# Kernel tuning notes

Measured on AMD Instinct MI355X. Metric: run time of the kernel, lower is better.

Reference implementation:

```python
import jax, jax.numpy as jnp
import numpy as np

# Tsit5 Butcher tableau (Tsitouras 2011), b7 = 0 for the accepted solution.
_C = (0.161, 0.327, 0.9, 0.9800255409045097, 1.0)
_A = (
    (0.161,),
    (-0.008480655492356989, 0.335480655492357),
    (2.8971530571054935, -6.359448489975075, 4.3622954328695815),
    (5.325864828439257, -11.748883564062828, 7.4955393428898365, -0.09249506636175525),
    (5.86145544294642, -12.92096931784711, 8.159367898576159, -0.071584973281401, -0.028269050394068383),
)
_B = (0.09646076681806523, 0.01, 0.4798896504144996, 1.379008574103742, -3.290069515436081, 2.324710524099774)

K_STEPS, BATCH, N_STATE, N_INPUT, HIDDEN = 512, 64, 128, 32, 256


def setup_inputs() -> dict:
    key = jax.random.key(0)
    k1, k2, k3, k4 = jax.random.split(key, 4)
    ts = jnp.linspace(0.0, 1.0, K_STEPS, dtype=jnp.float32)
    y0 = jax.random.normal(k1, (BATCH, N_STATE), dtype=jnp.float32)
    us = jax.random.normal(k2, (BATCH, K_STEPS, N_INPUT), dtype=jnp.float32)
    fan_in = 1 + N_STATE + N_INPUT  # t, y, u
    W1 = jax.random.normal(k3, (HIDDEN, fan_in), dtype=jnp.float32) / np.sqrt(fan_in)
    b1 = jnp.zeros((HIDDEN,), dtype=jnp.float32)
    W2 = jax.random.normal(k4, (N_STATE, HIDDEN), dtype=jnp.float32) / np.sqrt(HIDDEN)
    b2 = jnp.zeros((N_STATE,), dtype=jnp.float32)
    return {"ts": ts, "y0": y0, "us": us, "W1": W1, "b1": b1, "W2": W2, "b2": b2}


def _solve(ts, y0_i, us_i, W1, b1, W2, b2):
    """Integrate one trajectory with fixed-step Tsit5 on the save grid."""
    dt_grid = jnp.diff(ts)                              # (k-1,)
    # backward-Hermite derivative estimates for the input signal u(t)
    d = jnp.diff(us_i, axis=0) / dt_grid[:, None]       # (k-1, m)
    d = jnp.concatenate([d[:1], d], axis=0)             # (k, m)

    def func(t, y, u):
        z = jnp.concatenate([t[None], y, u])
        return W2 @ jnp.tanh(W1 @ z + b1) + b2

    def u_at(i, theta):
        # cubic Hermite interpolation of u on interval [ts[i], ts[i+1]]
        h = dt_grid[i]
        u0, u1, d0, d1 = us_i[i], us_i[i + 1], d[i], d[i + 1]
        t2 = theta * theta
        t3 = t2 * theta
        return ((2 * t3 - 3 * t2 + 1) * u0 + (t3 - 2 * t2 + theta) * h * d0
                + (-2 * t3 + 3 * t2) * u1 + (t3 - t2) * h * d1)

    def step(y, i):
        t0, h = ts[i], dt_grid[i]
        ks = []
        k = func(t0, y, u_at(i, jnp.float32(0.0)))
        ks.append(k)
        for c, arow in zip(_C, _A):
            ytmp = y + h * sum(a * kj for a, kj in zip(arow, ks))
            ks.append(func(t0 + c * h, ytmp, u_at(i, jnp.float32(c))))
        y_new = y + h * sum(b * kj for b, kj in zip(_B, ks))
        return y_new, y_new

    _, ys = jax.lax.scan(step, y0_i, jnp.arange(ts.shape[0] - 1))
    return jnp.concatenate([y0_i[None], ys], axis=0)    # (k, n)


def reference(ts, y0, us, W1, b1, W2, b2):
    return jax.vmap(_solve, in_axes=(None, 0, 0, None, None, None, None))(
        ts, y0, us, W1, b1, W2, b2
    )
```

## Files before the change

### kernel.cpp

```cpp
#include <hip/hip_runtime.h>

namespace {

typedef _Float16 h2 __attribute__((ext_vector_type(2)));

constexpr int KSTEPS = 512;
constexpr int NSTATE = 128;
constexpr int NINPUT = 32;
constexpr int HID    = 256;
constexpr int FANIN  = 161;
constexpr int BATCH  = 64;
constexpr int CHUNK  = 64;
constexpr int NCH    = 8;

constexpr size_t WS_M  = 0;
constexpr size_t WS_C  = WS_M + (size_t)HID * HID * 2;
constexpr size_t WS_US = WS_C + HID * 4;
constexpr size_t WS_HB = WS_US + (size_t)BATCH * KSTEPS * NINPUT * 2;
constexpr size_t WS_T  = WS_HB + (size_t)BATCH * KSTEPS * HID * 2;

__device__ __forceinline__ float fdot2(h2 a, h2 b, float c) {
#if __has_builtin(__builtin_amdgcn_fdot2)
  return __builtin_amdgcn_fdot2(a, b, c, false);
#else
  return c + (float)a[0] * (float)b[0] + (float)a[1] * (float)b[1];
#endif
}

__device__ __forceinline__ float fast_tanh(float x) {
  float e2 = __builtin_amdgcn_exp2f(x * 2.8853900817779268f);
  float r  = __builtin_amdgcn_rcpf(e2 + 1.0f);
  return __builtin_fmaf(-2.0f, r, 1.0f);
}

template <int CTRL>
__device__ __forceinline__ float dpp_add(float x) {
  int y = __builtin_amdgcn_update_dpp(0, __float_as_int(x), CTRL, 0xF, 0xF, false);
  return x + __int_as_float(y);
}
__device__ __forceinline__ float red8(float x) {
  x = dpp_add<0xB1>(x);
  x = dpp_add<0x4E>(x);
  x = dpp_add<0x141>(x);
  return x;
}

#define BAR() __asm__ volatile("s_waitcnt lgkmcnt(0)\n\ts_barrier" ::: "memory")

union F4 { float4 f; h2 h[4]; };

__global__ __launch_bounds__(256)
void k1_compose(const float* __restrict__ W1, const float* __restrict__ W2,
                const float* __restrict__ b2, _Float16* __restrict__ wsM,
                float* __restrict__ wsC) {
  const int j  = blockIdx.x;
  const int hc = threadIdx.x;
  const float* w1row = W1 + (size_t)j * FANIN + 1;
  float acc = 0.0f;
  for (int o = 0; o < NSTATE; ++o)
    acc = __builtin_fmaf(w1row[o], W2[(size_t)o * HID + hc], acc);
  wsM[(size_t)j * HID + hc] = (_Float16)acc;
  if (hc == 0) {
    float ca = 0.0f;
    for (int o = 0; o < NSTATE; ++o) ca = __builtin_fmaf(w1row[o], b2[o], ca);
    wsC[j] = ca;
  }
}

__global__ __launch_bounds__(256)
void k1b_transcode(const float* __restrict__ us, _Float16* __restrict__ us16) {
  const size_t idx = ((size_t)blockIdx.x * 256 + threadIdx.x) * 4;
  const float4 v = *(const float4*)(us + idx);
  us16[idx + 0] = (_Float16)v.x;
  us16[idx + 1] = (_Float16)v.y;
  us16[idx + 2] = (_Float16)v.z;
  us16[idx + 3] = (_Float16)v.w;
}

__global__ __launch_bounds__(256)
__attribute__((amdgpu_waves_per_eu(1, 1)))
void k2_main(const float* __restrict__ ts,
             const float* __restrict__ y0,
             const float* __restrict__ W1,
             const float* __restrict__ b1,
             char* __restrict__ ws)
{
  const int lt = threadIdx.x;
  const int g  = lt >> 3;
  const int kc = lt & 7;
  const int b  = blockIdx.x;

  const _Float16* wsM  = (const _Float16*)(ws + WS_M);
  const float*    wsC  = (const float*)(ws + WS_C);
  const _Float16* us16 = (const _Float16*)(ws + WS_US) + (size_t)b * KSTEPS * NINPUT;
  _Float16*       wsHB = (_Float16*)(ws + WS_HB) + (size_t)b * KSTEPS * HID;
  float*          wsT  = (float*)(ws + WS_T) + (size_t)b * NCH * HID;

  __shared__ __align__(16) _Float16 hbuf[2][320];
  __shared__ __align__(16) float y0s[NSTATE];
  __shared__ __align__(16) float tss[KSTEPS];
  __shared__ __align__(16) _Float16 usl[KSTEPS * NINPUT];

  {
    const F4* src = (const F4*)us16;
    F4* dst = (F4*)usl;
    #pragma unroll
    for (int it = 0; it < 8; ++it) dst[lt + 256 * it] = src[lt + 256 * it];
    tss[lt] = ts[lt];
    tss[lt + 256] = ts[lt + 256];
  }

  h2 w1m[8][16];
  #pragma unroll
  for (int r = 0; r < 8; ++r) {
    const F4* mp = (const F4*)(wsM + (size_t)(8 * g + r) * HID + 32 * kc);
    F4 m0 = mp[0], m1 = mp[1], m2 = mp[2], m3 = mp[3];
    #pragma unroll
    for (int i = 0; i < 4; ++i) {
      w1m[r][i]      = m0.h[i];
      w1m[r][4 + i]  = m1.h[i];
      w1m[r][8 + i]  = m2.h[i];
      w1m[r][12 + i] = m3.h[i];
    }
  }
  const float* w1row = W1 + (size_t)lt * FANIN;
  const float  w1t   = w1row[0];
  h2 w1u[16];
  #pragma unroll
  for (int i = 0; i < 16; ++i)
    w1u[i] = h2{(_Float16)w1row[129 + 2 * i], (_Float16)w1row[130 + 2 * i]};
  const float cR = wsC[lt];

  if (lt < NSTATE) y0s[lt] = y0[(size_t)b * NSTATE + lt];
  __syncthreads();
  float P = b1[lt];
  {
    const float* wy = w1row + 1;
    #pragma unroll 8
    for (int o = 0; o < NSTATE; ++o) P = __builtin_fmaf(wy[o], y0s[o], P);
  }

  constexpr double CcD[5] = {0.161, 0.327, 0.9, 0.9800255409045097, 1.0};
  constexpr float Af[5][5] = {
    {0.161f, 0.f, 0.f, 0.f, 0.f},
    {-0.008480655492356989f, 0.335480655492357f, 0.f, 0.f, 0.f},
    {2.8971530571054935f, -6.359448489975075f, 4.3622954328695815f, 0.f, 0.f},
    {5.325864828439257f, -11.748883564062828f, 7.4955393428898365f, -0.09249506636175525f, 0.f},
    {5.86145544294642f, -12.92096931784711f, 8.159367898576159f, -0.071584973281401f,
     -0.028269050394068383f}};
  constexpr float Bf[6] = {0.09646076681806523f, 0.01f, 0.4798896504144996f,
                           1.379008574103742f, -3.290069515436081f, 2.324710524099774f};

  float Ua, Ub = 0.0f, Uaprev = 0.0f, D = 0.0f;
  {
    const F4* up = (const F4*)(usl);
    F4 u0 = up[0], u1 = up[1], u2 = up[2], u3 = up[3];
    float s = 0.0f;
    #pragma unroll
    for (int i = 0; i < 4; ++i) {
      s = fdot2(w1u[i],      u0.h[i], s);
      s = fdot2(w1u[4 + i],  u1.h[i], s);
      s = fdot2(w1u[8 + i],  u2.h[i], s);
      s = fdot2(w1u[12 + i], u3.h[i], s);
    }
    Ua = s;
  }

  float tcur = ts[0], tn1 = ts[1];
  float dtp = 1.0f;
  const int slot = 40 * (lt >> 5) + (lt & 31);
  float h0v = fast_tanh(P + Ua + w1t * tcur);
  hbuf[0][slot] = (_Float16)h0v;
  float hB = Bf[0] * h0v;
  float Sacc = 0.0f;
  float aR[6];

  for (int i = 0; i < KSTEPS - 1; ++i) {
    const float dt = tn1 - tcur;
    const int   i2 = (i + 2 < KSTEPS) ? (i + 2) : (KSTEPS - 1);
    const float tn2 = tss[i2];
    F4 ur0, ur1, ur2, ur3;
    {
      const F4* up = (const F4*)(&usl[(i + 1) * NINPUT]);
      ur0 = up[0]; ur1 = up[1]; ur2 = up[2]; ur3 = up[3];
    }

    if (i > 0 && (i & (CHUNK - 1)) == 0)
      wsT[(size_t)(i >> 6) * HID + lt] = Sacc;

    #pragma unroll
    for (int e = 0; e < 6; ++e) {
      BAR();

      const F4* hp = (const F4*)(&hbuf[e & 1][40 * kc]);
      F4 hc0 = hp[0], hc1 = hp[1], hc2 = hp[2], hc3 = hp[3];

      if (e == 5) {
        wsHB[(size_t)i * HID + lt] = (_Float16)hB;
      }
      if (e == 0) {
        float s = 0.0f;
        #pragma unroll
        for (int q = 0; q < 4; ++q) {
          s = fdot2(w1u[q],      ur0.h[q], s);
          s = fdot2(w1u[4 + q],  ur1.h[q], s);
          s = fdot2(w1u[8 + q],  ur2.h[q], s);
          s = fdot2(w1u[12 + q], ur3.h[q], s);
        }
        Ub = s;
        D = (i == 0) ? (Ub - Ua)
                     : (Ua - Uaprev) * (dt * __builtin_amdgcn_rcpf(dtp));
      }

      float acc[8];
      #pragma unroll
      for (int r = 0; r < 8; ++r) {
        float a0 = fdot2(w1m[r][0], hc0.h[0], 0.0f);
        float a1 = fdot2(w1m[r][1], hc0.h[1], 0.0f);
        a0 = fdot2(w1m[r][2],  hc0.h[2], a0);
        a1 = fdot2(w1m[r][3],  hc0.h[3], a1);
        a0 = fdot2(w1m[r][4],  hc1.h[0], a0);
        a1 = fdot2(w1m[r][5],  hc1.h[1], a1);
        a0 = fdot2(w1m[r][6],  hc1.h[2], a0);
        a1 = fdot2(w1m[r][7],  hc1.h[3], a1);
        a0 = fdot2(w1m[r][8],  hc2.h[0], a0);
        a1 = fdot2(w1m[r][9],  hc2.h[1], a1);
        a0 = fdot2(w1m[r][10], hc2.h[2], a0);
        a1 = fdot2(w1m[r][11], hc2.h[3], a1);
        a0 = fdot2(w1m[r][12], hc3.h[0], a0);
        a1 = fdot2(w1m[r][13], hc3.h[1], a1);
        a0 = fdot2(w1m[r][14], hc3.h[2], a0);
        a1 = fdot2(w1m[r][15], hc3.h[3], a1);
        acc[r] = a0 + a1;
      }
      #pragma unroll
      for (int r = 0; r < 8; ++r) acc[r] = red8(acc[r]);
      float ae = acc[0];
      #pragma unroll
      for (int r = 1; r < 8; ++r) ae = (kc == r) ? acc[r] : ae;
      ae += cR;
      aR[e] = ae;

      if (e < 5) {
        float acm = 0.0f;
        #pragma unroll
        for (int mm = 0; mm <= e; ++mm) acm = __builtin_fmaf(Af[e][mm], aR[mm], acm);
        const double th = CcD[e];
        const float cu0 = (float)(th * th * th - 2.0 * th * th + 1.0);
        const float cu1 = (float)(2.0 * th * th - th * th * th);
        const float cd0 = (float)(th * th * th - 2.0 * th * th + th);
        const float ut  = cu0 * Ua + cu1 * Ub + cd0 * D;
        const float te  = __builtin_fmaf((float)th, dt, tcur);
        float pre = __builtin_fmaf(dt, acm, P) + ut;
        pre = __builtin_fmaf(w1t, te, pre);
        const float hv = fast_tanh(pre);
        hbuf[(e + 1) & 1][slot] = (_Float16)hv;
        hB = __builtin_fmaf(Bf[e + 1], hv, hB);
      } else {
        float acm = 0.0f;
        #pragma unroll
        for (int mm = 0; mm < 6; ++mm) acm = __builtin_fmaf(Bf[mm], aR[mm], acm);
        P = __builtin_fmaf(dt, acm, P);
        Sacc = __builtin_fmaf(dt, hB, Sacc);
        float pre = P + Ub;
        pre = __builtin_fmaf(w1t, tn1, pre);
        const float hv = fast_tanh(pre);
        hbuf[0][slot] = (_Float16)hv;
        hB = Bf[0] * hv;
      }
    }

    Uaprev = Ua; Ua = Ub;
    dtp = dt; tcur = tn1; tn1 = tn2;
  }
}

__global__ __launch_bounds__(256, 1)
void k4_out(const float* __restrict__ ts,
            const float* __restrict__ y0,
            const float* __restrict__ W2,
            const char* __restrict__ ws,
            float* __restrict__ out)
{
  const int blk = blockIdx.x;
  const int b = blk >> 3;
  const int c = blk & 7;
  const int lt = threadIdx.x;
  const int o    = lt >> 1;
  const int half = lt & 1;

  const _Float16* wsHB = (const _Float16*)(ws + WS_HB) + (size_t)b * KSTEPS * HID;
  const float*    wsT  = (const float*)(ws + WS_T) + (size_t)b * NCH * HID;
  float* outb = out + (size_t)b * KSTEPS * NSTATE;

  __shared__ __align__(16) _Float16 Sb[HID];

  h2 w2r[64];
  {
    const float* row = W2 + (size_t)o * HID + 128 * half;
    #pragma unroll
    for (int i = 0; i < 64; ++i)
      w2r[i] = h2{(_Float16)row[2 * i], (_Float16)row[2 * i + 1]};
  }
  const float y0o = y0[(size_t)b * NSTATE + o];
  if (c == 0 && lt < NSTATE) outb[lt] = y0[(size_t)b * NSTATE + lt];

  float S = (c > 0) ? wsT[(size_t)c * HID + lt] : 0.0f;
  const int i0 = c * CHUNK;
  const int n  = (KSTEPS - 1 - i0 < CHUNK) ? (KSTEPS - 1 - i0) : CHUNK;

  float tc = ts[i0], tn = ts[i0 + 1];
  float hcur = (float)wsHB[(size_t)i0 * HID + lt];
  for (int l = 0; l < n; ++l) {
    const int i = i0 + l;
    const int inx = (i + 1 < KSTEPS - 1) ? (i + 1) : (KSTEPS - 2);
    const float hnext = (float)wsHB[(size_t)inx * HID + lt];
    const float tnn = ts[(i + 2 < KSTEPS) ? (i + 2) : (KSTEPS - 1)];

    const float dt = tn - tc;
    S = __builtin_fmaf(dt, hcur, S);
    Sb[lt] = (_Float16)S;
    __syncthreads();

    const F4* sp = (const F4*)(&Sb[128 * half]);
    float v0 = 0.0f, v1 = 0.0f;
    #pragma unroll
    for (int q = 0; q < 16; ++q) {
      F4 sc = sp[q];
      v0 = fdot2(w2r[4 * q + 0], sc.h[0], v0);
      v1 = fdot2(w2r[4 * q + 1], sc.h[1], v1);
      v0 = fdot2(w2r[4 * q + 2], sc.h[2], v0);
      v1 = fdot2(w2r[4 * q + 3], sc.h[3], v1);
    }
    float v = v0 + v1;
    v += __shfl_xor(v, 1);
    if (half == 0) outb[(size_t)(i + 1) * NSTATE + o] = y0o + v;
    __syncthreads();

    hcur = hnext; tc = tn; tn = tnn;
  }
}

}

extern "C" void kernel_launch(void* const* d_in, const int* in_sizes, int n_in,
                              void* d_out, int out_size, void* d_ws, size_t ws_size,
                              hipStream_t stream) {
  const float* ts = (const float*)d_in[0];
  const float* y0 = (const float*)d_in[1];
  const float* us = (const float*)d_in[2];
  const float* W1 = (const float*)d_in[3];
  const float* b1 = (const float*)d_in[4];
  const float* W2 = (const float*)d_in[5];
  const float* b2 = (const float*)d_in[6];
  float* out = (float*)d_out;
  char* ws = (char*)d_ws;

  _Float16* wsM  = (_Float16*)(ws + WS_M);
  float*    wsC  = (float*)(ws + WS_C);
  _Float16* us16 = (_Float16*)(ws + WS_US);

  hipLaunchKernelGGL(k1_compose, dim3(HID), dim3(HID), 0, stream, W1, W2, b2, wsM, wsC);
  hipLaunchKernelGGL(k1b_transcode, dim3(BATCH * KSTEPS * NINPUT / 1024), dim3(256),
                     0, stream, us, us16);
  hipLaunchKernelGGL(k2_main, dim3(BATCH), dim3(256), 0, stream, ts, y0, W1, b1, ws);
  hipLaunchKernelGGL(k4_out, dim3(BATCH * NCH), dim3(256), 0, stream, ts, y0, W2,
                     (const char*)ws, out);
}
```

Before: 1.573 ms.

## Replace fdot2 matvec and DPP reduction with MFMA 16x16x32 f16 tiles

The per-stage 256x256 hidden-to-hidden matvec is moved from packed fdot2 dot products plus an 8-lane DPP reduction onto MFMA 16x16x32 f16 instructions. Each wave keeps four 16-row A tiles of the composed matrix in registers and broadcasts the hidden vector as the B operand. Thread-to-hidden-unit mapping is remapped so each lane extracts its own output element from the accumulator without a cross-lane reduction. This wastes 15 of 16 MFMA columns, since only one vector is multiplied, and the MFMA latency sits on the serial critical path between barriers.

After: 1.546 ms. Within noise of the previous version (-1.7%).

```diff
diff --git a/kernel.cpp b/kernel.cpp
--- a/kernel.cpp
+++ b/kernel.cpp
@@ -3,6 +3,8 @@
 namespace {
 
 typedef _Float16 h2 __attribute__((ext_vector_type(2)));
+typedef _Float16 f16x8 __attribute__((ext_vector_type(8)));
+typedef float    f32x4 __attribute__((ext_vector_type(4)));
 
 constexpr int KSTEPS = 512;
 constexpr int NSTATE = 128;
@@ -31,18 +33,6 @@
   float e2 = __builtin_amdgcn_exp2f(x * 2.8853900817779268f);
   float r  = __builtin_amdgcn_rcpf(e2 + 1.0f);
   return __builtin_fmaf(-2.0f, r, 1.0f);
-}
-
-template <int CTRL>
-__device__ __forceinline__ float dpp_add(float x) {
-  int y = __builtin_amdgcn_update_dpp(0, __float_as_int(x), CTRL, 0xF, 0xF, false);
-  return x + __int_as_float(y);
-}
-__device__ __forceinline__ float red8(float x) {
-  x = dpp_add<0xB1>(x);
-  x = dpp_add<0x4E>(x);
-  x = dpp_add<0x141>(x);
-  return x;
 }
 
 #define BAR() __asm__ volatile("s_waitcnt lgkmcnt(0)\n\ts_barrier" ::: "memory")
@@ -86,8 +76,10 @@
              char* __restrict__ ws)
 {
   const int lt = threadIdx.x;
-  const int g  = lt >> 3;
-  const int kc = lt & 7;
+  const int w  = lt >> 6;
+  const int ln = lt & 63;
+  const int klo = ((ln >> 4) & 3) * 8;
+  const int j  = 64 * w + 16 * ((ln >> 2) & 3) + 4 * (ln >> 4) + (ln & 3);
   const int b  = blockIdx.x;
 
   const _Float16* wsM  = (const _Float16*)(ws + WS_M);
@@ -96,7 +88,7 @@
   _Float16*       wsHB = (_Float16*)(ws + WS_HB) + (size_t)b * KSTEPS * HID;
   float*          wsT  = (float*)(ws + WS_T) + (size_t)b * NCH * HID;
 
-  __shared__ __align__(16) _Float16 hbuf[2][320];
+  __shared__ __align__(16) _Float16 hbuf[2][HID];
   __shared__ __align__(16) float y0s[NSTATE];
   __shared__ __align__(16) float tss[KSTEPS];
   __shared__ __align__(16) _Float16 usl[KSTEPS * NINPUT];
@@ -110,30 +102,26 @@
     tss[lt + 256] = ts[lt + 256];
   }
 
-  h2 w1m[8][16];
+  f16x8 af[4][8];
   #pragma unroll
-  for (int r = 0; r < 8; ++r) {
-    const F4* mp = (const F4*)(wsM + (size_t)(8 * g + r) * HID + 32 * kc);
-    F4 m0 = mp[0], m1 = mp[1], m2 = mp[2], m3 = mp[3];
-    #pragma unroll
-    for (int i = 0; i < 4; ++i) {
-      w1m[r][i]      = m0.h[i];
-      w1m[r][4 + i]  = m1.h[i];
-      w1m[r][8 + i]  = m2.h[i];
-      w1m[r][12 + i] = m3.h[i];
-    }
-  }
-  const float* w1row = W1 + (size_t)lt * FANIN;
+  for (int t = 0; t < 4; ++t) {
+    const int row = 64 * w + 16 * t + (ln & 15);
+    #pragma unroll
+    for (int kk = 0; kk < 8; ++kk)
+      af[t][kk] = *(const f16x8*)(wsM + (size_t)row * HID + kk * 32 + klo);
+  }
+
+  const float* w1row = W1 + (size_t)j * FANIN;
   const float  w1t   = w1row[0];
   h2 w1u[16];
   #pragma unroll
   for (int i = 0; i < 16; ++i)
     w1u[i] = h2{(_Float16)w1row[129 + 2 * i], (_Float16)w1row[130 + 2 * i]};
-  const float cR = wsC[lt];
+  const float cR = wsC[j];
 
   if (lt < NSTATE) y0s[lt] = y0[(size_t)b * NSTATE + lt];
   __syncthreads();
-  float P = b1[lt];
+  float P = b1[j];
   {
     const float* wy = w1row + 1;
     #pragma unroll 8
@@ -168,9 +156,8 @@
 
   float tcur = ts[0], tn1 = ts[1];
   float dtp = 1.0f;
-  const int slot = 40 * (lt >> 5) + (lt & 31);
   float h0v = fast_tanh(P + Ua + w1t * tcur);
-  hbuf[0][slot] = (_Float16)h0v;
+  hbuf[0][j] = (_Float16)h0v;
   float hB = Bf[0] * h0v;
   float Sacc = 0.0f;
   float aR[6];
@@ -186,17 +173,14 @@
     }
 
     if (i > 0 && (i & (CHUNK - 1)) == 0)
-      wsT[(size_t)(i >> 6) * HID + lt] = Sacc;
+      wsT[(size_t)(i >> 6) * HID + j] = Sacc;
 
     #pragma unroll
     for (int e = 0; e < 6; ++e) {
       BAR();
 
-      const F4* hp = (const F4*)(&hbuf[e & 1][40 * kc]);
-      F4 hc0 = hp[0], hc1 = hp[1], hc2 = hp[2], hc3 = hp[3];
-
       if (e == 5) {
-        wsHB[(size_t)i * HID + lt] = (_Float16)hB;
+        wsHB[(size_t)i * HID + j] = (_Float16)hB;
       }
       if (e == 0) {
         float s = 0.0f;
@@ -212,32 +196,31 @@
                      : (Ua - Uaprev) * (dt * __builtin_amdgcn_rcpf(dtp));
       }
 
-      float acc[8];
+      const _Float16* hb = hbuf[e & 1];
+      f32x4 ac0 = {0.f, 0.f, 0.f, 0.f};
+      f32x4 ac1 = {0.f, 0.f, 0.f, 0.f};
+      f32x4 ac2 = {0.f, 0.f, 0.f, 0.f};
+      f32x4 ac3 = {0.f, 0.f, 0.f, 0.f};
       #pragma unroll
-      for (int r = 0; r < 8; ++r) {
-        float a0 = fdot2(w1m[r][0], hc0.h[0], 0.0f);
-        float a1 = fdot2(w1m[r][1], hc0.h[1], 0.0f);
-        a0 = fdot2(w1m[r][2],  hc0.h[2], a0);
-        a1 = fdot2(w1m[r][3],  hc0.h[3], a1);
-        a0 = fdot2(w1m[r][4],  hc1.h[0], a0);
-        a1 = fdot2(w1m[r][5],  hc1.h[1], a1);
-        a0 = fdot2(w1m[r][6],  hc1.h[2], a0);
-        a1 = fdot2(w1m[r][7],  hc1.h[3], a1);
-        a0 = fdot2(w1m[r][8],  hc2.h[0], a0);
-        a1 = fdot2(w1m[r][9],  hc2.h[1], a1);
-        a0 = fdot2(w1m[r][10], hc2.h[2], a0);
-        a1 = fdot2(w1m[r][11], hc2.h[3], a1);
-        a0 = fdot2(w1m[r][12], hc3.h[0], a0);
-        a1 = fdot2(w1m[r][13], hc3.h[1], a1);
-        a0 = fdot2(w1m[r][14], hc3.h[2], a0);
-        a1 = fdot2(w1m[r][15], hc3.h[3], a1);
-        acc[r] = a0 + a1;
-      }
-      #pragma unroll
-      for (int r = 0; r < 8; ++r) acc[r] = red8(acc[r]);
-      float ae = acc[0];
-      #pragma unroll
-      for (int r = 1; r < 8; ++r) ae = (kc == r) ? acc[r] : ae;
+      for (int kk = 0; kk < 8; ++kk) {
+        const f16x8 bf = *(const f16x8*)(hb + kk * 32 + klo);
+        ac0 = __builtin_amdgcn_mfma_f32_16x16x32_f16(af[0][kk], bf, ac0, 0, 0, 0);
+        ac1 = __builtin_amdgcn_mfma_f32_16x16x32_f16(af[1][kk], bf, ac1, 0, 0, 0);
+        ac2 = __builtin_amdgcn_mfma_f32_16x16x32_f16(af[2][kk], bf, ac2, 0, 0, 0);
+        ac3 = __builtin_amdgcn_mfma_f32_16x16x32_f16(af[3][kk], bf, ac3, 0, 0, 0);
+      }
+      float ae;
+      {
+        const bool b0 = (ln & 1) != 0;
+        const bool b1s = (ln & 2) != 0;
+        float e0 = b1s ? (b0 ? ac0[3] : ac0[2]) : (b0 ? ac0[1] : ac0[0]);
+        float e1 = b1s ? (b0 ? ac1[3] : ac1[2]) : (b0 ? ac1[1] : ac1[0]);
+        float e2 = b1s ? (b0 ? ac2[3] : ac2[2]) : (b0 ? ac2[1] : ac2[0]);
+        float e3 = b1s ? (b0 ? ac3[3] : ac3[2]) : (b0 ? ac3[1] : ac3[0]);
+        const bool t0 = (ln & 4) != 0;
+        const bool t1 = (ln & 8) != 0;
+        ae = t1 ? (t0 ? e3 : e2) : (t0 ? e1 : e0);
+      }
       ae += cR;
       aR[e] = ae;
 
@@ -254,7 +237,7 @@
         float pre = __builtin_fmaf(dt, acm, P) + ut;
         pre = __builtin_fmaf(w1t, te, pre);
         const float hv = fast_tanh(pre);
-        hbuf[(e + 1) & 1][slot] = (_Float16)hv;
+        hbuf[(e + 1) & 1][j] = (_Float16)hv;
         hB = __builtin_fmaf(Bf[e + 1], hv, hB);
       } else {
         float acm = 0.0f;
@@ -265,7 +248,7 @@
         float pre = P + Ub;
         pre = __builtin_fmaf(w1t, tn1, pre);
         const float hv = fast_tanh(pre);
-        hbuf[0][slot] = (_Float16)hv;
+        hbuf[0][j] = (_Float16)hv;
         hB = Bf[0] * hv;
       }
     }
```
